# Kernel tuning notes

Measured on AMD Instinct MI355X. Metric: run time of the kernel, lower is better.

## Reference

```python
import jax, jax.numpy as jnp
import numpy as np

B, L, H, NUM_LABELS = 4, 256, 768, 13


def setup_inputs() -> dict:
    key = jax.random.key(0)
    k1, k2, k3, k4, k5 = jax.random.split(key, 5)
    s1 = 1.0 / np.sqrt(2 * H)
    s2 = 1.0 / np.sqrt(H)
    return {
        "hidden_states": jax.random.normal(k1, (B, L, H), dtype=jnp.float32),
        "W1": jax.random.uniform(k2, (2 * H, H), jnp.float32, -s1, s1),
        "b1": jax.random.uniform(k3, (H,), jnp.float32, -s1, s1),
        "W2": jax.random.uniform(k4, (H, NUM_LABELS), jnp.float32, -s2, s2),
        "b2": jax.random.uniform(k5, (NUM_LABELS,), jnp.float32, -s2, s2),
    }


def reference(hidden_states, W1, b1, W2, b2):
    # Original: ffn(cat([x_start expand over dim2, x_end expand over dim1], -1))
    # Algebraically: Linear(2H->H) on the concat == proj(x_start) + proj(x_end)
    # broadcast over the L x L span grid, avoiding the (B,L,L,2H) tensor.
    H_ = hidden_states.shape[-1]
    xs_proj = jnp.einsum('bsh,hk->bsk', hidden_states, W1[:H_])   # start half
    xe_proj = jnp.einsum('bsh,hk->bsk', hidden_states, W1[H_:])   # end half
    h = xs_proj[:, :, None, :] + xe_proj[:, None, :, :] + b1      # (B,L,L,H)
    h = jax.nn.gelu(h, approximate=False)                         # torch GELU default = exact erf
    logits = jnp.einsum('bijk,kn->bijn', h, W2) + b2              # (B,L,L,num_labels)
    return logits
```

## Files before the change

kernel.cpp:

```cpp
#include <hip/hip_runtime.h>
#include <math.h>

#define H 768
#define L 256
#define NB 4
#define NL 13

typedef _Float16 h2 __attribute__((ext_vector_type(2)));
typedef _Float16 h4 __attribute__((ext_vector_type(4)));
typedef _Float16 half8 __attribute__((ext_vector_type(8)));
typedef float f32x4 __attribute__((ext_vector_type(4)));

__device__ inline h2 gelu_pk(h2 x) {
    const _Float16 kC = (_Float16)3.75f;
    h2 hi = {kC, kC}, lo = {(_Float16)-3.75f, (_Float16)-3.75f};
    h2 xc = __builtin_elementwise_min(__builtin_elementwise_max(x, lo), hi);
    h2 u = xc * xc;
    const _Float16 d4v = (_Float16)2.0333e-5f,  d3v = (_Float16)-0.00084672f;
    const _Float16 d2v = (_Float16)0.0140002f,  d1v = (_Float16)-0.1234557f;
    const _Float16 d0v = (_Float16)0.7946463f;
    h2 d4 = {d4v, d4v}, d3 = {d3v, d3v}, d2 = {d2v, d2v}, d1 = {d1v, d1v}, d0 = {d0v, d0v};
    h2 p = u * (u * (u * (u * d4 + d3) + d2) + d1) + d0;
    h2 t = xc * p;
    h2 w = x * t + x;
    const _Float16 kH = (_Float16)0.5f;
    h2 halfv = {kH, kH};
    return w * halfv;
}

__global__ __launch_bounds__(256) void gemm_fused(
    const float* __restrict__ X, const float* __restrict__ W1,
    const float* __restrict__ b1, const float* __restrict__ W2,
    _Float16* __restrict__ Pxs2, _Float16* __restrict__ Pxe,
    _Float16* __restrict__ Bfrag2)
{
    const int tid = threadIdx.x;

    if (blockIdx.y == 24) {
        int base = blockIdx.x * 768 + tid;
        #pragma unroll
        for (int r = 0; r < 3; ++r) {
            int idx = base + r * 256;
            int u = idx & 7;
            int lane = (idx >> 3) & 63;
            int kb = idx >> 9;
            int k = kb * 32 + ((lane >> 4) << 3) + u;
            int n = lane & 15;
            float v = (n < NL) ? W2[(size_t)k * NL + n] : 0.f;
            Bfrag2[idx] = (_Float16)v;
        }
        return;
    }

    __shared__ _Float16 As[64][72];
    __shared__ _Float16 Bs[64][72];
    const int w = tid >> 6, lane = tid & 63;
    const int ln = lane & 15, quad = lane >> 4;
    const int m0 = blockIdx.x * 64;
    const int n0g = blockIdx.y * 64;
    const bool isE = (n0g >= H);
    const float* Wb = W1 + (isE ? (size_t)H * H : 0);
    const int c0 = isE ? (n0g - H) : n0g;

    const int ar = tid >> 4;
    const int ac = (tid & 15) * 4;
    const int bc = (tid & 15) * 4;

    f32x4 acc[2][2] = {};
    for (int kr = 0; kr < H / 64; ++kr) {
        const int k0 = kr * 64;
        #pragma unroll
        for (int r = 0; r < 4; ++r) {
            int arow = r * 16 + ar;
            float4 f = *(const float4*)&X[(size_t)(m0 + arow) * H + k0 + ac];
            h4 o = { (_Float16)f.x, (_Float16)f.y, (_Float16)f.z, (_Float16)f.w };
            *(h4*)&As[arow][ac] = o;
        }
        #pragma unroll
        for (int r = 0; r < 2; ++r) {
            int kpl = r * 16 + (tid >> 4);
            const float* wr = &Wb[(size_t)(k0 + 2 * kpl) * H + c0 + bc];
            float4 fa = *(const float4*)wr;
            float4 fb = *(const float4*)(wr + H);
            h2 p0 = {(_Float16)fa.x, (_Float16)fb.x};
            h2 p1 = {(_Float16)fa.y, (_Float16)fb.y};
            h2 p2 = {(_Float16)fa.z, (_Float16)fb.z};
            h2 p3 = {(_Float16)fa.w, (_Float16)fb.w};
            *(h2*)&Bs[bc + 0][2 * kpl] = p0;
            *(h2*)&Bs[bc + 1][2 * kpl] = p1;
            *(h2*)&Bs[bc + 2][2 * kpl] = p2;
            *(h2*)&Bs[bc + 3][2 * kpl] = p3;
        }
        __syncthreads();
        #pragma unroll
        for (int sub = 0; sub < 2; ++sub) {
            const int ko = sub * 32 + quad * 8;
            half8 a0 = *(const half8*)&As[(w & 1) * 32 + ln][ko];
            half8 a1 = *(const half8*)&As[(w & 1) * 32 + 16 + ln][ko];
            half8 b0 = *(const half8*)&Bs[(w >> 1) * 32 + ln][ko];
            half8 b1f = *(const half8*)&Bs[(w >> 1) * 32 + 16 + ln][ko];
            acc[0][0] = __builtin_amdgcn_mfma_f32_16x16x32_f16(a0, b0, acc[0][0], 0, 0, 0);
            acc[0][1] = __builtin_amdgcn_mfma_f32_16x16x32_f16(a0, b1f, acc[0][1], 0, 0, 0);
            acc[1][0] = __builtin_amdgcn_mfma_f32_16x16x32_f16(a1, b0, acc[1][0], 0, 0, 0);
            acc[1][1] = __builtin_amdgcn_mfma_f32_16x16x32_f16(a1, b1f, acc[1][1], 0, 0, 0);
        }
        __syncthreads();
    }

    const int mb = m0 + (w & 1) * 32;
    const int nb = (w >> 1) * 32;
    if (!isE) {
        float bv[2] = { b1[n0g + nb + ln], b1[n0g + nb + 16 + ln] };
        #pragma unroll
        for (int mt = 0; mt < 2; ++mt)
            #pragma unroll
            for (int nt = 0; nt < 2; ++nt) {
                int n = n0g + nb + nt * 16 + ln;
                #pragma unroll
                for (int r = 0; r < 4; ++r) {
                    int m = mb + mt * 16 + quad * 4 + r;
                    Pxs2[(size_t)m * H + n] = (_Float16)(acc[mt][nt][r] + bv[nt]);
                }
            }
    } else {
        #pragma unroll
        for (int mt = 0; mt < 2; ++mt)
            #pragma unroll
            for (int nt = 0; nt < 2; ++nt) {
                int n = c0 + nb + nt * 16 + ln;
                #pragma unroll
                for (int r = 0; r < 4; ++r) {
                    int m = mb + mt * 16 + quad * 4 + r;
                    Pxe[(size_t)m * H + n] = (_Float16)acc[mt][nt][r];
                }
            }
    }
}

__global__ __launch_bounds__(256, 3) void span_mfma_kernel(
    const _Float16* __restrict__ Pxs2, const _Float16* __restrict__ Pxe,
    const _Float16* __restrict__ Bfrag2, const float* __restrict__ b2,
    float* __restrict__ out)
{
    __shared__ unsigned int xsf[4 * H / 2];
    const int ip = blockIdx.x >> 2;
    const int jq = blockIdx.x & 3;
    const int bi0 = ip * 4;
    const int b = bi0 >> 8;
    const int tid = threadIdx.x;

    const unsigned int* xsrc = (const unsigned int*)(Pxs2 + (size_t)bi0 * H);
    #pragma unroll
    for (int t = 0; t < 6; ++t) xsf[t * 256 + tid] = xsrc[t * 256 + tid];

    const int wave = tid >> 6;
    const int lane = tid & 63;
    const int n = lane & 15;
    const int quad = lane >> 4;
    const int j_load = jq * 64 + wave * 16 + n;

    const _Float16* xerow = Pxe + (size_t)(b * L + j_load) * H + quad * 8;
    const half8* bptr = (const half8*)(Bfrag2 + (size_t)lane * 8);

    f32x4 acc[4] = {};
    __syncthreads();

    uint4 xe0 = *(const uint4*)(xerow);
    uint4 xe1 = *(const uint4*)(xerow + 32);

    #pragma unroll 3
    for (int kb = 0; kb < H / 32; ++kb) {
        uint4 xecur = xe0;
        xe0 = xe1;
        if (kb < H / 32 - 2)
            xe1 = *(const uint4*)(xerow + (kb + 2) * 32);

        half8 bfrag = bptr[kb * 64];
        h2 xep[4] = { __builtin_bit_cast(h2, xecur.x), __builtin_bit_cast(h2, xecur.y),
                      __builtin_bit_cast(h2, xecur.z), __builtin_bit_cast(h2, xecur.w) };
        const int xo = kb * 16 + quad * 4;

        #pragma unroll
        for (int i01 = 0; i01 < 4; ++i01) {
            uint4 xsd = *(const uint4*)&xsf[i01 * (H / 2) + xo];
            h2 xsp[4] = { __builtin_bit_cast(h2, xsd.x), __builtin_bit_cast(h2, xsd.y),
                          __builtin_bit_cast(h2, xsd.z), __builtin_bit_cast(h2, xsd.w) };
            unsigned int pk[4];
            #pragma unroll
            for (int p = 0; p < 4; ++p) {
                h2 g = gelu_pk(xsp[p] + xep[p]);
                pk[p] = __builtin_bit_cast(unsigned int, g);
            }
            uint4 pk4 = {pk[0], pk[1], pk[2], pk[3]};
            half8 afrag = __builtin_bit_cast(half8, pk4);
            acc[i01] = __builtin_amdgcn_mfma_f32_16x16x32_f16(afrag, bfrag, acc[i01], 0, 0, 0);
        }
    }

    if (n < NL) {
        float b2v = b2[n];
        #pragma unroll
        for (int i01 = 0; i01 < 4; ++i01)
            #pragma unroll
            for (int r = 0; r < 4; ++r) {
                int j = jq * 64 + wave * 16 + quad * 4 + r;
                out[((size_t)(bi0 + i01) * L + j) * NL + n] = acc[i01][r] + b2v;
            }
    }
}

extern "C" void kernel_launch(void* const* d_in, const int* in_sizes, int n_in,
                              void* d_out, int out_size, void* d_ws, size_t ws_size,
                              hipStream_t stream)
{
    (void)in_sizes; (void)n_in; (void)out_size; (void)ws_size;
    const float* X  = (const float*)d_in[0];
    const float* W1 = (const float*)d_in[1];
    const float* b1 = (const float*)d_in[2];
    const float* W2 = (const float*)d_in[3];
    const float* b2 = (const float*)d_in[4];
    float* out = (float*)d_out;

    char* ws = (char*)d_ws;
    _Float16* Pxs2   = (_Float16*)ws;
    _Float16* Pxe    = Pxs2 + (size_t)NB * L * H;
    _Float16* Bfrag2 = Pxe + (size_t)NB * L * H;

    gemm_fused<<<dim3(16, 25), 256, 0, stream>>>(X, W1, b1, W2, Pxs2, Pxe, Bfrag2);
    span_mfma_kernel<<<NB * L, 256, 0, stream>>>(Pxs2, Pxe, Bfrag2, b2, out);
}
```

Measured before the change: 123.7 us.

## Split span kernel K across waves, double-buffer projection GEMM with smaller tiles

The projection GEMM now uses 32x64 tiles on a flat 1D grid of 784 blocks, with register-staged double-buffered shared memory so global loads for the next K slice overlap the MFMA work on the current one. The span kernel doubles its block count: each block covers 32 j values, and its four waves split the K dimension in halves, combining partial accumulators through shared memory. W2 fragments are also prefetched into registers two steps ahead. The aim is more parallelism and better latency hiding on a small grid, at the cost of a reduction step, an extra barrier and more shared memory per block.

```diff
diff --git a/kernel.cpp b/kernel.cpp
--- a/kernel.cpp
+++ b/kernel.cpp
@@ -36,8 +36,8 @@
 {
     const int tid = threadIdx.x;
 
-    if (blockIdx.y == 24) {
-        int base = blockIdx.x * 768 + tid;
+    if (blockIdx.x >= 768) {
+        int base = (blockIdx.x - 768) * 768 + tid;
         #pragma unroll
         for (int r = 0; r < 3; ++r) {
             int idx = base + r * 256;
@@ -45,106 +45,119 @@
             int lane = (idx >> 3) & 63;
             int kb = idx >> 9;
             int k = kb * 32 + ((lane >> 4) << 3) + u;
-            int n = lane & 15;
-            float v = (n < NL) ? W2[(size_t)k * NL + n] : 0.f;
+            int nn = lane & 15;
+            float v = (nn < NL) ? W2[(size_t)k * NL + nn] : 0.f;
             Bfrag2[idx] = (_Float16)v;
         }
         return;
     }
 
-    __shared__ _Float16 As[64][72];
-    __shared__ _Float16 Bs[64][72];
+    __shared__ _Float16 As[2][32][72];
+    __shared__ _Float16 Bs[2][64][72];
+
     const int w = tid >> 6, lane = tid & 63;
     const int ln = lane & 15, quad = lane >> 4;
-    const int m0 = blockIdx.x * 64;
-    const int n0g = blockIdx.y * 64;
+    const int bm = blockIdx.x & 31;
+    const int bn = blockIdx.x >> 5;
+    const int m0 = bm * 32;
+    const int n0g = bn * 64;
     const bool isE = (n0g >= H);
     const float* Wb = W1 + (isE ? (size_t)H * H : 0);
     const int c0 = isE ? (n0g - H) : n0g;
 
     const int ar = tid >> 4;
     const int ac = (tid & 15) * 4;
-    const int bc = (tid & 15) * 4;
-
-    f32x4 acc[2][2] = {};
-    for (int kr = 0; kr < H / 64; ++kr) {
-        const int k0 = kr * 64;
-        #pragma unroll
-        for (int r = 0; r < 4; ++r) {
-            int arow = r * 16 + ar;
-            float4 f = *(const float4*)&X[(size_t)(m0 + arow) * H + k0 + ac];
-            h4 o = { (_Float16)f.x, (_Float16)f.y, (_Float16)f.z, (_Float16)f.w };
-            *(h4*)&As[arow][ac] = o;
-        }
-        #pragma unroll
-        for (int r = 0; r < 2; ++r) {
-            int kpl = r * 16 + (tid >> 4);
-            const float* wr = &Wb[(size_t)(k0 + 2 * kpl) * H + c0 + bc];
-            float4 fa = *(const float4*)wr;
-            float4 fb = *(const float4*)(wr + H);
-            h2 p0 = {(_Float16)fa.x, (_Float16)fb.x};
-            h2 p1 = {(_Float16)fa.y, (_Float16)fb.y};
-            h2 p2 = {(_Float16)fa.z, (_Float16)fb.z};
-            h2 p3 = {(_Float16)fa.w, (_Float16)fb.w};
-            *(h2*)&Bs[bc + 0][2 * kpl] = p0;
-            *(h2*)&Bs[bc + 1][2 * kpl] = p1;
-            *(h2*)&Bs[bc + 2][2 * kpl] = p2;
-            *(h2*)&Bs[bc + 3][2 * kpl] = p3;
-        }
-        __syncthreads();
+
+    float4 fA0, fA1, fB0a, fB0b, fB1a, fB1b;
+
+#define G_LOAD(KR) do { \
+    const int k0_ = (KR) * 64; \
+    fA0 = *(const float4*)&X[(size_t)(m0 + ar) * H + k0_ + ac]; \
+    fA1 = *(const float4*)&X[(size_t)(m0 + 16 + ar) * H + k0_ + ac]; \
+    const float* wr0_ = &Wb[(size_t)(k0_ + 2 * ar) * H + c0 + ac]; \
+    fB0a = *(const float4*)wr0_; \
+    fB0b = *(const float4*)(wr0_ + H); \
+    const float* wr1_ = &Wb[(size_t)(k0_ + 2 * (16 + ar)) * H + c0 + ac]; \
+    fB1a = *(const float4*)wr1_; \
+    fB1b = *(const float4*)(wr1_ + H); \
+} while (0)
+
+#define L_STORE(BUF) do { \
+    h4 oa0 = { (_Float16)fA0.x, (_Float16)fA0.y, (_Float16)fA0.z, (_Float16)fA0.w }; \
+    h4 oa1 = { (_Float16)fA1.x, (_Float16)fA1.y, (_Float16)fA1.z, (_Float16)fA1.w }; \
+    *(h4*)&As[BUF][ar][ac] = oa0; \
+    *(h4*)&As[BUF][16 + ar][ac] = oa1; \
+    h2 p0 = {(_Float16)fB0a.x, (_Float16)fB0b.x}; \
+    h2 p1 = {(_Float16)fB0a.y, (_Float16)fB0b.y}; \
+    h2 p2 = {(_Float16)fB0a.z, (_Float16)fB0b.z}; \
+    h2 p3 = {(_Float16)fB0a.w, (_Float16)fB0b.w}; \
+    *(h2*)&Bs[BUF][ac + 0][2 * ar] = p0; \
+    *(h2*)&Bs[BUF][ac + 1][2 * ar] = p1; \
+    *(h2*)&Bs[BUF][ac + 2][2 * ar] = p2; \
+    *(h2*)&Bs[BUF][ac + 3][2 * ar] = p3; \
+    h2 q0 = {(_Float16)fB1a.x, (_Float16)fB1b.x}; \
+    h2 q1 = {(_Float16)fB1a.y, (_Float16)fB1b.y}; \
+    h2 q2 = {(_Float16)fB1a.z, (_Float16)fB1b.z}; \
+    h2 q3 = {(_Float16)fB1a.w, (_Float16)fB1b.w}; \
+    *(h2*)&Bs[BUF][ac + 0][2 * (16 + ar)] = q0; \
+    *(h2*)&Bs[BUF][ac + 1][2 * (16 + ar)] = q1; \
+    *(h2*)&Bs[BUF][ac + 2][2 * (16 + ar)] = q2; \
+    *(h2*)&Bs[BUF][ac + 3][2 * (16 + ar)] = q3; \
+} while (0)
+
+    const int wm = w & 1, wn = w >> 1;
+    f32x4 acc[2] = {};
+
+    G_LOAD(0);
+    L_STORE(0);
+    __syncthreads();
+
+    for (int kr = 0; kr < 12; ++kr) {
+        const int cur = kr & 1;
+        if (kr < 11) G_LOAD(kr + 1);
         #pragma unroll
         for (int sub = 0; sub < 2; ++sub) {
             const int ko = sub * 32 + quad * 8;
-            half8 a0 = *(const half8*)&As[(w & 1) * 32 + ln][ko];
-            half8 a1 = *(const half8*)&As[(w & 1) * 32 + 16 + ln][ko];
-            half8 b0 = *(const half8*)&Bs[(w >> 1) * 32 + ln][ko];
-            half8 b1f = *(const half8*)&Bs[(w >> 1) * 32 + 16 + ln][ko];
-            acc[0][0] = __builtin_amdgcn_mfma_f32_16x16x32_f16(a0, b0, acc[0][0], 0, 0, 0);
-            acc[0][1] = __builtin_amdgcn_mfma_f32_16x16x32_f16(a0, b1f, acc[0][1], 0, 0, 0);
-            acc[1][0] = __builtin_amdgcn_mfma_f32_16x16x32_f16(a1, b0, acc[1][0], 0, 0, 0);
-            acc[1][1] = __builtin_amdgcn_mfma_f32_16x16x32_f16(a1, b1f, acc[1][1], 0, 0, 0);
-        }
+            half8 a   = *(const half8*)&As[cur][wm * 16 + ln][ko];
+            half8 b0  = *(const half8*)&Bs[cur][wn * 32 + ln][ko];
+            half8 b1f = *(const half8*)&Bs[cur][wn * 32 + 16 + ln][ko];
+            acc[0] = __builtin_amdgcn_mfma_f32_16x16x32_f16(a, b0,  acc[0], 0, 0, 0);
+            acc[1] = __builtin_amdgcn_mfma_f32_16x16x32_f16(a, b1f, acc[1], 0, 0, 0);
+        }
+        if (kr < 11) L_STORE(cur ^ 1);
         __syncthreads();
     }
 
-    const int mb = m0 + (w & 1) * 32;
-    const int nb = (w >> 1) * 32;
+    const int mb = m0 + wm * 16 + quad * 4;
+    const int nb = wn * 32;
     if (!isE) {
-        float bv[2] = { b1[n0g + nb + ln], b1[n0g + nb + 16 + ln] };
-        #pragma unroll
-        for (int mt = 0; mt < 2; ++mt)
-            #pragma unroll
-            for (int nt = 0; nt < 2; ++nt) {
-                int n = n0g + nb + nt * 16 + ln;
-                #pragma unroll
-                for (int r = 0; r < 4; ++r) {
-                    int m = mb + mt * 16 + quad * 4 + r;
-                    Pxs2[(size_t)m * H + n] = (_Float16)(acc[mt][nt][r] + bv[nt]);
-                }
-            }
+        float bv0 = b1[n0g + nb + ln];
+        float bv1 = b1[n0g + nb + 16 + ln];
+        #pragma unroll
+        for (int r = 0; r < 4; ++r) {
+            Pxs2[(size_t)(mb + r) * H + (n0g + nb + ln)]      = (_Float16)(acc[0][r] + bv0);
+            Pxs2[(size_t)(mb + r) * H + (n0g + nb + 16 + ln)] = (_Float16)(acc[1][r] + bv1);
+        }
     } else {
         #pragma unroll
-        for (int mt = 0; mt < 2; ++mt)
-            #pragma unroll
-            for (int nt = 0; nt < 2; ++nt) {
-                int n = c0 + nb + nt * 16 + ln;
-                #pragma unroll
-                for (int r = 0; r < 4; ++r) {
-                    int m = mb + mt * 16 + quad * 4 + r;
-                    Pxe[(size_t)m * H + n] = (_Float16)acc[mt][nt][r];
-                }
-            }
-    }
-}
-
-__global__ __launch_bounds__(256, 3) void span_mfma_kernel(
+        for (int r = 0; r < 4; ++r) {
+            Pxe[(size_t)(mb + r) * H + (c0 + nb + ln)]      = (_Float16)acc[0][r];
+            Pxe[(size_t)(mb + r) * H + (c0 + nb + 16 + ln)] = (_Float16)acc[1][r];
+        }
+    }
+#undef G_LOAD
+#undef L_STORE
+}
+
+__global__ __launch_bounds__(256, 6) void span_mfma_kernel(
     const _Float16* __restrict__ Pxs2, const _Float16* __restrict__ Pxe,
     const _Float16* __restrict__ Bfrag2, const float* __restrict__ b2,
     float* __restrict__ out)
 {
     __shared__ unsigned int xsf[4 * H / 2];
-    const int ip = blockIdx.x >> 2;
-    const int jq = blockIdx.x & 3;
+    __shared__ f32x4 redbuf[2][4][64];
+    const int ip = blockIdx.x >> 3;
+    const int jq = blockIdx.x & 7;
     const int bi0 = ip * 4;
     const int b = bi0 >> 8;
     const int tid = threadIdx.x;
@@ -153,11 +166,16 @@
     #pragma unroll
     for (int t = 0; t < 6; ++t) xsf[t * 256 + tid] = xsrc[t * 256 + tid];
 
-    const int wave = tid >> 6;
+    const int w = tid >> 6;
     const int lane = tid & 63;
+    const int jh = w & 1;
+    const int kh = w >> 1;
     const int n = lane & 15;
     const int quad = lane >> 4;
-    const int j_load = jq * 64 + wave * 16 + n;
+    const int j_load = jq * 32 + jh * 16 + n;
+
+    const int kb0 = kh * 12;
+    const int kbe = kb0 + 12;
 
     const _Float16* xerow = Pxe + (size_t)(b * L + j_load) * H + quad * 8;
     const half8* bptr = (const half8*)(Bfrag2 + (size_t)lane * 8);
@@ -165,17 +183,21 @@
     f32x4 acc[4] = {};
     __syncthreads();
 
-    uint4 xe0 = *(const uint4*)(xerow);
-    uint4 xe1 = *(const uint4*)(xerow + 32);
+    uint4 xe0 = *(const uint4*)(xerow + kb0 * 32);
+    uint4 xe1 = *(const uint4*)(xerow + (kb0 + 1) * 32);
+    uint4 bf0 = *(const uint4*)(bptr + (size_t)kb0 * 64);
+    uint4 bf1 = *(const uint4*)(bptr + (size_t)(kb0 + 1) * 64);
 
     #pragma unroll 3
-    for (int kb = 0; kb < H / 32; ++kb) {
-        uint4 xecur = xe0;
-        xe0 = xe1;
-        if (kb < H / 32 - 2)
+    for (int kb = kb0; kb < kbe; ++kb) {
+        uint4 xecur = xe0;  xe0 = xe1;
+        uint4 bfcur = bf0;  bf0 = bf1;
+        if (kb + 2 < kbe) {
             xe1 = *(const uint4*)(xerow + (kb + 2) * 32);
-
-        half8 bfrag = bptr[kb * 64];
+            bf1 = *(const uint4*)(bptr + (size_t)(kb + 2) * 64);
+        }
+
+        half8 bfrag = __builtin_bit_cast(half8, bfcur);
         h2 xep[4] = { __builtin_bit_cast(h2, xecur.x), __builtin_bit_cast(h2, xecur.y),
                       __builtin_bit_cast(h2, xecur.z), __builtin_bit_cast(h2, xecur.w) };
         const int xo = kb * 16 + quad * 4;
@@ -197,15 +219,23 @@
         }
     }
 
-    if (n < NL) {
+    if (kh == 1) {
+        #pragma unroll
+        for (int i01 = 0; i01 < 4; ++i01) redbuf[jh][i01][lane] = acc[i01];
+    }
+    __syncthreads();
+
+    if (kh == 0 && n < NL) {
         float b2v = b2[n];
         #pragma unroll
-        for (int i01 = 0; i01 < 4; ++i01)
+        for (int i01 = 0; i01 < 4; ++i01) {
+            f32x4 r2 = redbuf[jh][i01][lane];
             #pragma unroll
             for (int r = 0; r < 4; ++r) {
-                int j = jq * 64 + wave * 16 + quad * 4 + r;
-                out[((size_t)(bi0 + i01) * L + j) * NL + n] = acc[i01][r] + b2v;
+                int j = jq * 32 + jh * 16 + quad * 4 + r;
+                out[((size_t)(bi0 + i01) * L + j) * NL + n] = acc[i01][r] + r2[r] + b2v;
             }
+        }
     }
 }
 
@@ -226,6 +256,6 @@
     _Float16* Pxe    = Pxs2 + (size_t)NB * L * H;
     _Float16* Bfrag2 = Pxe + (size_t)NB * L * H;
 
-    gemm_fused<<<dim3(16, 25), 256, 0, stream>>>(X, W1, b1, W2, Pxs2, Pxe, Bfrag2);
-    span_mfma_kernel<<<NB * L, 256, 0, stream>>>(Pxs2, Pxe, Bfrag2, b2, out);
-}
+    gemm_fused<<<dim3(784), 256, 0, stream>>>(X, W1, b1, W2, Pxs2, Pxe, Bfrag2);
+    span_mfma_kernel<<<dim3(2048), 256, 0, stream>>>(Pxs2, Pxe, Bfrag2, b2, out);
+}
```

Measured after the change: 123.6 us. Within noise of the previous version (-0.0%).
